# Optimization experiments

Measured on AMD Instinct MI355X. Metric: run time of the kernel, lower is better.

The kernel has to match this reference:

```python
import jax, jax.numpy as jnp
import numpy as np

B, N, D, E, K = 4, 4096, 768, 8, 2
H = 4 * D
LN_EPS = 1e-5


def setup_inputs() -> dict:
    key = jax.random.key(0)
    ks = jax.random.split(key, 9)
    s_d = 1.0 / np.sqrt(D)
    s_h = 1.0 / np.sqrt(H)
    return {
        "x": jax.random.normal(ks[0], (B, N, D), dtype=jnp.float32),
        "router_w": jax.random.normal(ks[1], (D, E), dtype=jnp.float32) * s_d,
        "router_b": jnp.zeros((E,), dtype=jnp.float32),
        "w1": jax.random.normal(ks[2], (E, D, H), dtype=jnp.float32) * s_d,
        "b1": jnp.zeros((E, H), dtype=jnp.float32),
        "w2": jax.random.normal(ks[3], (E, H, D), dtype=jnp.float32) * s_h,
        "b2": jnp.zeros((E, D), dtype=jnp.float32),
        "gamma": jnp.ones((D,), dtype=jnp.float32),
        "beta": jnp.zeros((D,), dtype=jnp.float32),
    }


def reference(x, router_w, router_b, w1, b1, w2, b2, gamma, beta):
    # Router logits and top-k gating (softmax over top-k values, in fp32)
    logits = jnp.einsum("bnd,de->bne", x, router_w) + router_b
    topv, topi = jax.lax.top_k(logits, K)                       # [B,N,K]
    w = jax.nn.softmax(topv.astype(jnp.float32), axis=-1).astype(x.dtype)
    # Per-token per-expert combine weight: [B,N,E]
    onehot = (topi[..., None] == jnp.arange(E)).astype(x.dtype)  # [B,N,K,E]
    we = jnp.einsum("bnk,bnke->bne", w, onehot)
    # Dense per-expert FFN, weighted combine (loop over small fixed E)
    out = jnp.zeros_like(x)
    for e in range(E):
        h = jax.nn.gelu(jnp.einsum("bnd,dh->bnh", x, w1[e]) + b1[e],
                        approximate=False)                      # exact GELU like torch
        y_e = jnp.einsum("bnh,hd->bnd", h, w2[e]) + b2[e]
        out = out + y_e * we[..., e:e + 1]
    # Residual + LayerNorm
    y = x + out
    mu = jnp.mean(y, axis=-1, keepdims=True)
    var = jnp.mean((y - mu) ** 2, axis=-1, keepdims=True)
    return (y - mu) * jax.lax.rsqrt(var + LN_EPS) * gamma + beta
```

## Files before the change

kernel.cpp:

```cpp
#include <hip/hip_runtime.h>
#include <hip/hip_bf16.h>
#include <math.h>

#define T_TOK 16384
#define DIM 768
#define NE 8
#define HID 3072
#define PADT 33792
#define CHUNK_CAP 16896
#define NSLOT (T_TOK * 2)

typedef unsigned short u16;
typedef __attribute__((ext_vector_type(8))) short bf16x8;
typedef __attribute__((ext_vector_type(4))) float f32x4;

__device__ __forceinline__ u16 f2bf(float f) {
  union { float f; unsigned u; } v; v.f = f;
  unsigned r = v.u + 0x7FFF + ((v.u >> 16) & 1);
  return (u16)(r >> 16);
}

__device__ __forceinline__ float bf2f(u16 u) {
  union { unsigned u; float f; } v; v.u = ((unsigned)u) << 16; return v.f;
}

__device__ __forceinline__ void async16(void* lds, const void* g) {
  __builtin_amdgcn_global_load_lds((const __attribute__((address_space(1))) void*)g,
                                   (__attribute__((address_space(3))) void*)lds, 16, 0, 0);
}

__device__ __forceinline__ float gelu_f(float v) {
  float z = fabsf(v) * 0.70710678118f;
  float t = __builtin_amdgcn_rcpf(1.f + 0.3275911f * z);
  float p = t * (0.254829592f +
            t * (-0.284496736f +
            t * (1.421413741f +
            t * (-1.453152027f +
            t * 1.061405429f))));
  float e = __expf(-z * z);
  float erfz = fmaf(-p, e, 1.f);
  float s = copysignf(erfz, v);
  return 0.5f * v * (1.f + s);
}

__global__ __launch_bounds__(256) void transpose_cvt(const float* __restrict__ in,
                                                     u16* __restrict__ outp, int R, int C) {
  __shared__ float tile[32][33];
  int e = blockIdx.z;
  int c0 = blockIdx.x * 32, r0 = blockIdx.y * 32;
  int tx = threadIdx.x & 31, ty = threadIdx.x >> 5;
  const float* ip = in + (size_t)e * R * C;
  u16* op = outp + (size_t)e * R * C;
#pragma unroll
  for (int i = 0; i < 4; ++i)
    tile[ty + i * 8][tx] = ip[(size_t)(r0 + ty + i * 8) * C + c0 + tx];
  __syncthreads();
#pragma unroll
  for (int i = 0; i < 4; ++i)
    op[(size_t)(c0 + ty + i * 8) * R + r0 + tx] = f2bf(tile[tx][ty + i * 8]);
}

__global__ __launch_bounds__(256) void router_kernel(
    const float* __restrict__ x, const float* __restrict__ rw,
    const float* __restrict__ rb, int* __restrict__ idxb,
    float* __restrict__ wtb, u16* __restrict__ xb) {
  __shared__ float rwt[NE * DIM];
  for (int i = threadIdx.x; i < NE * DIM; i += 256) {
    int d = i >> 3, e = i & 7;
    rwt[e * DIM + d] = rw[i];
  }
  __syncthreads();
  int lane = threadIdx.x & 63, wv = threadIdx.x >> 6;
#pragma unroll 1
  for (int it = 0; it < 8; ++it) {
    int t = blockIdx.x * 32 + wv * 8 + it;
    const float4* xr = (const float4*)(x + (size_t)t * DIM);
    float4 xv[3];
#pragma unroll
    for (int i = 0; i < 3; ++i) xv[i] = xr[lane + i * 64];
    ushort4* xo = (ushort4*)(xb + (size_t)t * DIM);
#pragma unroll
    for (int i = 0; i < 3; ++i)
      xo[lane + i * 64] = make_ushort4(f2bf(xv[i].x), f2bf(xv[i].y), f2bf(xv[i].z), f2bf(xv[i].w));
    float acc[NE];
#pragma unroll
    for (int e = 0; e < NE; ++e) acc[e] = 0.f;
#pragma unroll
    for (int i = 0; i < 3; ++i) {
#pragma unroll
      for (int e = 0; e < NE; ++e) {
        float4 w4 = ((const float4*)(rwt + e * DIM))[lane + i * 64];
        acc[e] += xv[i].x * w4.x + xv[i].y * w4.y + xv[i].z * w4.z + xv[i].w * w4.w;
      }
    }
#pragma unroll
    for (int e = 0; e < NE; ++e)
      for (int off = 32; off; off >>= 1) acc[e] += __shfl_down(acc[e], off);
    if (lane == 0) {
      float lg[NE];
#pragma unroll
      for (int e = 0; e < NE; ++e) lg[e] = acc[e] + rb[e];
      int i0 = 0;
#pragma unroll
      for (int e = 1; e < NE; ++e) if (lg[e] > lg[i0]) i0 = e;
      int i1 = -1;
#pragma unroll
      for (int e = 0; e < NE; ++e)
        if (e != i0 && (i1 < 0 || lg[e] > lg[i1])) i1 = e;
      float ee = expf(lg[i1] - lg[i0]);
      float w0 = 1.f / (1.f + ee);
      float w1 = ee / (1.f + ee);
      idxb[t * 2] = i0; idxb[t * 2 + 1] = i1;
      wtb[t * 2] = w0; wtb[t * 2 + 1] = w1;
    }
  }
}

__global__ __launch_bounds__(256) void hist_kernel(const int* __restrict__ idxb,
                                                   int* __restrict__ whist) {
  int wv = threadIdx.x >> 6, lane = threadIdx.x & 63;
  int g = blockIdx.x * 4 + wv;
  int cnt = 0;
#pragma unroll
  for (int j = 0; j < 2; ++j) {
    int e = idxb[g * 128 + j * 64 + lane];
#pragma unroll
    for (int ex = 0; ex < NE; ++ex) {
      unsigned long long m = __ballot(e == ex);
      if (lane == ex) cnt += __popcll(m);
    }
  }
  if (lane < NE) whist[g * NE + lane] = cnt;
}

__global__ __launch_bounds__(256) void scan_kernel(const int* __restrict__ whist,
                                                   int* __restrict__ gbase,
                                                   int* __restrict__ offsets,
                                                   int* __restrict__ counts) {
  __shared__ int sgb[256 * NE];
  __shared__ int tot[NE], soff[NE + 1];
  int tid = threadIdx.x;
  if (tid < NE) {
    int run = 0;
    for (int g = 0; g < 256; ++g) { sgb[g * NE + tid] = run; run += whist[g * NE + tid]; }
    tot[tid] = run; counts[tid] = run;
  }
  __syncthreads();
  if (tid == 0) {
    int off = 0;
    for (int e = 0; e < NE; ++e) {
      soff[e] = off; offsets[e] = off;
      off += (tot[e] + 127) & ~127;
    }
    soff[NE] = off; offsets[NE] = off;
  }
  __syncthreads();
  for (int i = tid; i < 256 * NE; i += 256) gbase[i] = sgb[i] + soff[i & 7];
}

__global__ __launch_bounds__(256) void scatter_kernel(
    const int* __restrict__ idxb, const int* __restrict__ gbase,
    int* __restrict__ g_tok, int* __restrict__ pairpos) {
  int wv = threadIdx.x >> 6, lane = threadIdx.x & 63;
  int g = blockIdx.x * 4 + wv;
  int run = (lane < NE) ? gbase[g * NE + lane] : 0;
  unsigned long long ltm = (1ull << lane) - 1ull;
#pragma unroll
  for (int j = 0; j < 2; ++j) {
    int slot = g * 128 + j * 64 + lane;
    int e = idxb[slot];
    int myrank = 0;
#pragma unroll
    for (int ex = 0; ex < NE; ++ex) {
      unsigned long long m = __ballot(e == ex);
      int b = __shfl(run, ex);
      if (e == ex) myrank = b + __popcll(m & ltm);
      if (lane == ex) run += __popcll(m);
    }
    g_tok[myrank] = slot >> 1;
    pairpos[slot] = myrank;
  }
}

__global__ __launch_bounds__(256, 2) void gemm1_kernel(
    const u16* __restrict__ xb, const u16* __restrict__ w1t,
    const float* __restrict__ b1, const int* __restrict__ g_tok,
    const int* __restrict__ offsets, const int* __restrict__ counts,
    u16* __restrict__ hbuf, int g0) {
  const int g = g0 + blockIdx.y * 128;
  int e = -1;
#pragma unroll
  for (int i = 0; i < NE; ++i)
    if (g >= offsets[i] && g < offsets[i + 1]) e = i;
  if (e < 0) return;
  const int off = offsets[e];
  const int cnt = counts[e];
  const int r0 = g - off;
  if (r0 >= cnt) return;
  const int n0 = blockIdx.x * 128;

  __shared__ u16 As[2][128 * 64];
  __shared__ u16 Bs[2][128 * 64];

  const int tid = threadIdx.x;
  const int lane = tid & 63;
  const int wv = tid >> 6;
  const int wr = wv >> 1, wc = wv & 1;
  const int scol = (((lane & 7) ^ (lane >> 3)) * 8);

  const u16* agp[4];
  const u16* bgp[4];
#pragma unroll
  for (int i = 0; i < 4; ++i) {
    int r = r0 + wv * 32 + i * 8 + (lane >> 3);
    int rr = r < cnt ? r : cnt - 1;
    int tok = g_tok[off + rr];
    agp[i] = xb + (size_t)tok * DIM + scol;
    int n = n0 + wv * 32 + i * 8 + (lane >> 3);
    bgp[i] = w1t + ((size_t)e * HID + n) * DIM + scol;
  }

  f32x4 acc[4][4];
#pragma unroll
  for (int i = 0; i < 4; ++i)
#pragma unroll
    for (int j = 0; j < 4; ++j) acc[i][j] = (f32x4){0.f, 0.f, 0.f, 0.f};

  const int NT = DIM / 64;
#pragma unroll
  for (int i = 0; i < 4; ++i) {
    async16(&As[0][(wv * 32 + i * 8) * 64], agp[i]);
    async16(&Bs[0][(wv * 32 + i * 8) * 64], bgp[i]);
  }
#pragma unroll 1
  for (int t = 0; t < NT; ++t) {
    const int cur = t & 1;
    if (t + 1 < NT) {
      const int nxt = cur ^ 1;
      const int kt = (t + 1) * 64;
#pragma unroll
      for (int i = 0; i < 4; ++i) {
        async16(&As[nxt][(wv * 32 + i * 8) * 64], agp[i] + kt);
        async16(&Bs[nxt][(wv * 32 + i * 8) * 64], bgp[i] + kt);
      }
      asm volatile("s_waitcnt vmcnt(8)" ::: "memory");
    } else {
      asm volatile("s_waitcnt vmcnt(0)" ::: "memory");
    }
    __builtin_amdgcn_s_barrier();
    __builtin_amdgcn_s_setprio(1);
#pragma unroll
    for (int kk = 0; kk < 2; ++kk) {
      bf16x8 af[4], bfr[4];
#pragma unroll
      for (int i = 0; i < 4; ++i)
        af[i] = *(const bf16x8*)&As[cur][(wr * 64 + i * 16 + (lane & 15)) * 64 +
                                        (((kk * 4 + (lane >> 4)) ^ (lane & 7)) * 8)];
#pragma unroll
      for (int j = 0; j < 4; ++j)
        bfr[j] = *(const bf16x8*)&Bs[cur][(wc * 64 + j * 16 + (lane & 15)) * 64 +
                                         (((kk * 4 + (lane >> 4)) ^ (lane & 7)) * 8)];
#pragma unroll
      for (int i = 0; i < 4; ++i)
#pragma unroll
        for (int j = 0; j < 4; ++j)
          acc[i][j] = __builtin_amdgcn_mfma_f32_16x16x32_bf16(af[i], bfr[j], acc[i][j], 0, 0, 0);
    }
    __builtin_amdgcn_s_setprio(0);
    asm volatile("" ::: "memory");
    __builtin_amdgcn_s_barrier();
  }

#pragma unroll
  for (int i = 0; i < 4; ++i) {
#pragma unroll
    for (int j = 0; j < 4; ++j) {
      int col = n0 + wc * 64 + j * 16 + (lane & 15);
      float bias = b1[e * HID + col];
#pragma unroll
      for (int rg = 0; rg < 4; ++rg) {
        int rloc = wr * 64 + i * 16 + (lane >> 4) * 4 + rg;
        if (r0 + rloc < cnt) {
          float v = gelu_f(acc[i][j][rg] + bias);
          hbuf[(size_t)(g - g0 + rloc) * HID + col] = f2bf(v);
        }
      }
    }
  }
}

__global__ __launch_bounds__(256, 2) void gemm2_kernel(
    const u16* __restrict__ hbuf, const u16* __restrict__ w2t,
    const float* __restrict__ b2, const int* __restrict__ offsets,
    const int* __restrict__ counts, u16* __restrict__ ygb, int g0) {
  const int g = g0 + blockIdx.y * 128;
  int e = -1;
#pragma unroll
  for (int i = 0; i < NE; ++i)
    if (g >= offsets[i] && g < offsets[i + 1]) e = i;
  if (e < 0) return;
  const int off = offsets[e];
  const int cnt = counts[e];
  const int r0 = g - off;
  if (r0 >= cnt) return;
  const int n0 = blockIdx.x * 128;

  __shared__ u16 As[2][128 * 64];
  __shared__ u16 Bs[2][128 * 64];

  const int tid = threadIdx.x;
  const int lane = tid & 63;
  const int wv = tid >> 6;
  const int wr = wv >> 1, wc = wv & 1;
  const int scol = (((lane & 7) ^ (lane >> 3)) * 8);

  const u16* agp[4];
  const u16* bgp[4];
#pragma unroll
  for (int i = 0; i < 4; ++i) {
    int r = r0 + wv * 32 + i * 8 + (lane >> 3);
    int rr = r < cnt ? r : cnt - 1;
    agp[i] = hbuf + (size_t)(off + rr - g0) * HID + scol;
    int n = n0 + wv * 32 + i * 8 + (lane >> 3);
    bgp[i] = w2t + ((size_t)e * DIM + n) * HID + scol;
  }

  f32x4 acc[4][4];
#pragma unroll
  for (int i = 0; i < 4; ++i)
#pragma unroll
    for (int j = 0; j < 4; ++j) acc[i][j] = (f32x4){0.f, 0.f, 0.f, 0.f};

  const int NT = HID / 64;
#pragma unroll
  for (int i = 0; i < 4; ++i) {
    async16(&As[0][(wv * 32 + i * 8) * 64], agp[i]);
    async16(&Bs[0][(wv * 32 + i * 8) * 64], bgp[i]);
  }
#pragma unroll 1
  for (int t = 0; t < NT; ++t) {
    const int cur = t & 1;
    if (t + 1 < NT) {
      const int nxt = cur ^ 1;
      const int kt = (t + 1) * 64;
#pragma unroll
      for (int i = 0; i < 4; ++i) {
        async16(&As[nxt][(wv * 32 + i * 8) * 64], agp[i] + kt);
        async16(&Bs[nxt][(wv * 32 + i * 8) * 64], bgp[i] + kt);
      }
      asm volatile("s_waitcnt vmcnt(8)" ::: "memory");
    } else {
      asm volatile("s_waitcnt vmcnt(0)" ::: "memory");
    }
    __builtin_amdgcn_s_barrier();
    __builtin_amdgcn_s_setprio(1);
#pragma unroll
    for (int kk = 0; kk < 2; ++kk) {
      bf16x8 af[4], bfr[4];
#pragma unroll
      for (int i = 0; i < 4; ++i)
        af[i] = *(const bf16x8*)&As[cur][(wr * 64 + i * 16 + (lane & 15)) * 64 +
                                        (((kk * 4 + (lane >> 4)) ^ (lane & 7)) * 8)];
#pragma unroll
      for (int j = 0; j < 4; ++j)
        bfr[j] = *(const bf16x8*)&Bs[cur][(wc * 64 + j * 16 + (lane & 15)) * 64 +
                                         (((kk * 4 + (lane >> 4)) ^ (lane & 7)) * 8)];
#pragma unroll
      for (int i = 0; i < 4; ++i)
#pragma unroll
        for (int j = 0; j < 4; ++j)
          acc[i][j] = __builtin_amdgcn_mfma_f32_16x16x32_bf16(af[i], bfr[j], acc[i][j], 0, 0, 0);
    }
    __builtin_amdgcn_s_setprio(0);
    asm volatile("" ::: "memory");
    __builtin_amdgcn_s_barrier();
  }

#pragma unroll
  for (int i = 0; i < 4; ++i) {
#pragma unroll
    for (int j = 0; j < 4; ++j) {
      int col = n0 + wc * 64 + j * 16 + (lane & 15);
      float bias = b2[e * DIM + col];
#pragma unroll
      for (int rg = 0; rg < 4; ++rg) {
        int rloc = wr * 64 + i * 16 + (lane >> 4) * 4 + rg;
        if (r0 + rloc < cnt)
          ygb[(size_t)(off + r0 + rloc) * DIM + col] = f2bf(acc[i][j][rg] + bias);
      }
    }
  }
}

__global__ __launch_bounds__(256) void combine_ln_kernel(
    const float* __restrict__ x, const u16* __restrict__ ygb,
    const int* __restrict__ pairpos, const float* __restrict__ wtb,
    const float* __restrict__ gamma, const float* __restrict__ beta,
    float* __restrict__ out) {
  int t = blockIdx.x;
  int p0 = pairpos[t * 2], p1 = pairpos[t * 2 + 1];
  float w0 = wtb[t * 2], w1 = wtb[t * 2 + 1];
  const float* xr = x + (size_t)t * DIM;
  const u16* y0 = ygb + (size_t)p0 * DIM;
  const u16* y1 = ygb + (size_t)p1 * DIM;
  float y[3];
  float s = 0.f, s2 = 0.f;
#pragma unroll
  for (int i = 0; i < 3; ++i) {
    int d = threadIdx.x + i * 256;
    float v = xr[d] + w0 * bf2f(y0[d]) + w1 * bf2f(y1[d]);
    y[i] = v; s += v; s2 += v * v;
  }
  for (int o = 32; o; o >>= 1) { s += __shfl_down(s, o); s2 += __shfl_down(s2, o); }
  __shared__ float red[8];
  int lane = threadIdx.x & 63, wv = threadIdx.x >> 6;
  if (lane == 0) { red[wv] = s; red[4 + wv] = s2; }
  __syncthreads();
  s = red[0] + red[1] + red[2] + red[3];
  s2 = red[4] + red[5] + red[6] + red[7];
  float mu = s * (1.f / DIM);
  float var = s2 * (1.f / DIM) - mu * mu;
  float inv = 1.f / sqrtf(var + 1e-5f);
#pragma unroll
  for (int i = 0; i < 3; ++i) {
    int d = threadIdx.x + i * 256;
    out[(size_t)t * DIM + d] = (y[i] - mu) * inv * gamma[d] + beta[d];
  }
}

extern "C" void kernel_launch(void* const* d_in, const int* in_sizes, int n_in,
                              void* d_out, int out_size, void* d_ws, size_t ws_size,
                              hipStream_t stream) {
  const float* x = (const float*)d_in[0];
  const float* rw = (const float*)d_in[1];
  const float* rb = (const float*)d_in[2];
  const float* w1 = (const float*)d_in[3];
  const float* b1 = (const float*)d_in[4];
  const float* w2 = (const float*)d_in[5];
  const float* b2 = (const float*)d_in[6];
  const float* gamma = (const float*)d_in[7];
  const float* beta = (const float*)d_in[8];
  float* out = (float*)d_out;

  char* p = (char*)d_ws;
  size_t o = 0;
  auto take = [&](size_t b) { void* q = (void*)(p + o); o += (b + 255) & ~((size_t)255); return q; };
  u16* xb = (u16*)take((size_t)T_TOK * DIM * 2);
  u16* w1t = (u16*)take((size_t)NE * HID * DIM * 2);
  u16* w2t = (u16*)take((size_t)NE * DIM * HID * 2);
  u16* ygb = (u16*)take((size_t)PADT * DIM * 2);
  int* g_tok = (int*)take((size_t)PADT * 4);
  int* pairpos = (int*)take((size_t)NSLOT * 4);
  int* idxb = (int*)take((size_t)NSLOT * 4);
  float* wtb = (float*)take((size_t)NSLOT * 4);
  int* whist = (int*)take((size_t)256 * NE * 4);
  int* gbase = (int*)take((size_t)256 * NE * 4);
  int* counts = (int*)take(64);
  int* offsets = (int*)take(64);
  (void)in_sizes; (void)n_in; (void)out_size;

  if (o + 256 > ws_size) return;
  size_t rem = ws_size - o;
  int chunk = (int)(rem / ((size_t)HID * 2));
  if (chunk > CHUNK_CAP) chunk = CHUNK_CAP;
  chunk &= ~127;
  if (chunk < 128) return;
  u16* hbuf = (u16*)take((size_t)chunk * HID * 2);

  router_kernel<<<512, 256, 0, stream>>>(x, rw, rb, idxb, wtb, xb);
  transpose_cvt<<<dim3(HID / 32, DIM / 32, NE), 256, 0, stream>>>(w1, w1t, DIM, HID);
  transpose_cvt<<<dim3(DIM / 32, HID / 32, NE), 256, 0, stream>>>(w2, w2t, HID, DIM);
  hist_kernel<<<64, 256, 0, stream>>>(idxb, whist);
  scan_kernel<<<1, 256, 0, stream>>>(whist, gbase, offsets, counts);
  scatter_kernel<<<64, 256, 0, stream>>>(idxb, gbase, g_tok, pairpos);
  for (int g0 = 0; g0 < PADT; g0 += chunk) {
    gemm1_kernel<<<dim3(HID / 128, chunk / 128), 256, 0, stream>>>(
        xb, w1t, b1, g_tok, offsets, counts, hbuf, g0);
    gemm2_kernel<<<dim3(DIM / 128, chunk / 128), 256, 0, stream>>>(
        hbuf, w2t, b2, offsets, counts, ygb, g0);
  }
  combine_ln_kernel<<<T_TOK, 256, 0, stream>>>(x, ygb, pairpos, wtb, gamma, beta, out);
}
```

Measured before the change: 704.5 us.

## Use 256x128 tiles with 8 waves and triple-buffered LDS pipeline in expert GEMMs

Both grouped GEMMs move from 128x128 tiles with 4 waves and double buffering to 256x128 tiles with 8 waves and a three-stage async LDS pipeline that prefetches two k-tiles ahead. B fragments are loaded once per k-tile and reused across the M sub-tiles. Expert padding becomes 256 rows and the hbuf chunk cap is raised so a single pass can cover the whole padded range. The intent is more reuse of weight tiles and more latency hiding. The cost is more LDS per block (144 KB), lower occupancy of 1 block per CU, and extra padded rows per expert.

```diff
diff --git a/kernel.cpp b/kernel.cpp
--- a/kernel.cpp
+++ b/kernel.cpp
@@ -6,8 +6,7 @@
 #define DIM 768
 #define NE 8
 #define HID 3072
-#define PADT 33792
-#define CHUNK_CAP 16896
+#define PADT 34816
 #define NSLOT (T_TOK * 2)
 
 typedef unsigned short u16;
@@ -150,7 +149,7 @@
     int off = 0;
     for (int e = 0; e < NE; ++e) {
       soff[e] = off; offsets[e] = off;
-      off += (tot[e] + 127) & ~127;
+      off += (tot[e] + 255) & ~255;
     }
     soff[NE] = off; offsets[NE] = off;
   }
@@ -182,43 +181,44 @@
   }
 }
 
-__global__ __launch_bounds__(256, 2) void gemm1_kernel(
+
+__global__ __launch_bounds__(512, 1) void gemm1_kernel(
     const u16* __restrict__ xb, const u16* __restrict__ w1t,
     const float* __restrict__ b1, const int* __restrict__ g_tok,
     const int* __restrict__ offsets, const int* __restrict__ counts,
     u16* __restrict__ hbuf, int g0) {
-  const int g = g0 + blockIdx.y * 128;
+  const int g = g0 + blockIdx.y * 256;
   int e = -1;
 #pragma unroll
   for (int i = 0; i < NE; ++i)
     if (g >= offsets[i] && g < offsets[i + 1]) e = i;
   if (e < 0) return;
-  const int off = offsets[e];
-  const int cnt = counts[e];
-  const int r0 = g - off;
+  const int off = offsets[e], cnt = counts[e], r0 = g - off;
   if (r0 >= cnt) return;
   const int n0 = blockIdx.x * 128;
 
-  __shared__ u16 As[2][128 * 64];
-  __shared__ u16 Bs[2][128 * 64];
+  __shared__ u16 As[3][256 * 64];
+  __shared__ u16 Bs[3][128 * 64];
 
   const int tid = threadIdx.x;
   const int lane = tid & 63;
-  const int wv = tid >> 6;
-  const int wr = wv >> 1, wc = wv & 1;
-  const int scol = (((lane & 7) ^ (lane >> 3)) * 8);
-
-  const u16* agp[4];
-  const u16* bgp[4];
+  const int w = tid >> 6;
+  const int wm = w >> 1;
+  const int wn = w & 1;
+  const int src = ((lane & 7) ^ (lane >> 3)) * 8;
+  const int lrow = w * 8 + (lane >> 3);
+
+  const u16* ap[4];
+  const u16* bp[2];
 #pragma unroll
   for (int i = 0; i < 4; ++i) {
-    int r = r0 + wv * 32 + i * 8 + (lane >> 3);
+    int r = r0 + i * 64 + lrow;
     int rr = r < cnt ? r : cnt - 1;
-    int tok = g_tok[off + rr];
-    agp[i] = xb + (size_t)tok * DIM + scol;
-    int n = n0 + wv * 32 + i * 8 + (lane >> 3);
-    bgp[i] = w1t + ((size_t)e * HID + n) * DIM + scol;
-  }
+    ap[i] = xb + (size_t)g_tok[off + rr] * DIM + src;
+  }
+#pragma unroll
+  for (int i = 0; i < 2; ++i)
+    bp[i] = w1t + ((size_t)e * HID + n0 + i * 64 + lrow) * DIM + src;
 
   f32x4 acc[4][4];
 #pragma unroll
@@ -227,103 +227,104 @@
     for (int j = 0; j < 4; ++j) acc[i][j] = (f32x4){0.f, 0.f, 0.f, 0.f};
 
   const int NT = DIM / 64;
-#pragma unroll
-  for (int i = 0; i < 4; ++i) {
-    async16(&As[0][(wv * 32 + i * 8) * 64], agp[i]);
-    async16(&Bs[0][(wv * 32 + i * 8) * 64], bgp[i]);
-  }
+  auto stage = [&](int buf, int kt) {
+#pragma unroll
+    for (int i = 0; i < 4; ++i)
+      async16(&As[buf][(i * 64 + w * 8) * 64], ap[i] + kt * 64);
+#pragma unroll
+    for (int i = 0; i < 2; ++i)
+      async16(&Bs[buf][(i * 64 + w * 8) * 64], bp[i] + kt * 64);
+  };
+  stage(0, 0);
+  stage(1, 1);
+  asm volatile("s_waitcnt vmcnt(6)" ::: "memory");
+  __builtin_amdgcn_s_barrier();
+
 #pragma unroll 1
   for (int t = 0; t < NT; ++t) {
-    const int cur = t & 1;
+    const int bc = t % 3;
+    if (t + 2 < NT) stage((t + 2) % 3, t + 2);
+    bf16x8 bfr[4][2];
+#pragma unroll
+    for (int nj = 0; nj < 4; ++nj)
+#pragma unroll
+      for (int kk = 0; kk < 2; ++kk)
+        bfr[nj][kk] = *(const bf16x8*)&Bs[bc][(wn * 64 + nj * 16 + (lane & 15)) * 64 +
+                                             (((kk * 4 + (lane >> 4)) ^ (lane & 7)) * 8)];
+    __builtin_amdgcn_s_setprio(1);
+#pragma unroll
+    for (int mi = 0; mi < 4; ++mi) {
+      bf16x8 af[2];
+#pragma unroll
+      for (int kk = 0; kk < 2; ++kk)
+        af[kk] = *(const bf16x8*)&As[bc][(wm * 64 + mi * 16 + (lane & 15)) * 64 +
+                                         (((kk * 4 + (lane >> 4)) ^ (lane & 7)) * 8)];
+#pragma unroll
+      for (int nj = 0; nj < 4; ++nj)
+#pragma unroll
+        for (int kk = 0; kk < 2; ++kk)
+          acc[mi][nj] = __builtin_amdgcn_mfma_f32_16x16x32_bf16(af[kk], bfr[nj][kk],
+                                                                acc[mi][nj], 0, 0, 0);
+    }
+    __builtin_amdgcn_s_setprio(0);
     if (t + 1 < NT) {
-      const int nxt = cur ^ 1;
-      const int kt = (t + 1) * 64;
-#pragma unroll
-      for (int i = 0; i < 4; ++i) {
-        async16(&As[nxt][(wv * 32 + i * 8) * 64], agp[i] + kt);
-        async16(&Bs[nxt][(wv * 32 + i * 8) * 64], bgp[i] + kt);
+      if (t + 2 < NT) asm volatile("s_waitcnt vmcnt(6)" ::: "memory");
+      else            asm volatile("s_waitcnt vmcnt(0)" ::: "memory");
+      __builtin_amdgcn_s_barrier();
+    }
+  }
+
+#pragma unroll
+  for (int mi = 0; mi < 4; ++mi)
+#pragma unroll
+    for (int nj = 0; nj < 4; ++nj) {
+      int col = n0 + wn * 64 + nj * 16 + (lane & 15);
+      float bias = b1[e * HID + col];
+#pragma unroll
+      for (int rg = 0; rg < 4; ++rg) {
+        int rloc = wm * 64 + mi * 16 + (lane >> 4) * 4 + rg;
+        if (r0 + rloc < cnt)
+          hbuf[(size_t)(g - g0 + rloc) * HID + col] = f2bf(gelu_f(acc[mi][nj][rg] + bias));
       }
-      asm volatile("s_waitcnt vmcnt(8)" ::: "memory");
-    } else {
-      asm volatile("s_waitcnt vmcnt(0)" ::: "memory");
-    }
-    __builtin_amdgcn_s_barrier();
-    __builtin_amdgcn_s_setprio(1);
-#pragma unroll
-    for (int kk = 0; kk < 2; ++kk) {
-      bf16x8 af[4], bfr[4];
-#pragma unroll
-      for (int i = 0; i < 4; ++i)
-        af[i] = *(const bf16x8*)&As[cur][(wr * 64 + i * 16 + (lane & 15)) * 64 +
-                                        (((kk * 4 + (lane >> 4)) ^ (lane & 7)) * 8)];
-#pragma unroll
-      for (int j = 0; j < 4; ++j)
-        bfr[j] = *(const bf16x8*)&Bs[cur][(wc * 64 + j * 16 + (lane & 15)) * 64 +
-                                         (((kk * 4 + (lane >> 4)) ^ (lane & 7)) * 8)];
-#pragma unroll
-      for (int i = 0; i < 4; ++i)
-#pragma unroll
-        for (int j = 0; j < 4; ++j)
-          acc[i][j] = __builtin_amdgcn_mfma_f32_16x16x32_bf16(af[i], bfr[j], acc[i][j], 0, 0, 0);
-    }
-    __builtin_amdgcn_s_setprio(0);
-    asm volatile("" ::: "memory");
-    __builtin_amdgcn_s_barrier();
-  }
-
-#pragma unroll
-  for (int i = 0; i < 4; ++i) {
-#pragma unroll
-    for (int j = 0; j < 4; ++j) {
-      int col = n0 + wc * 64 + j * 16 + (lane & 15);
-      float bias = b1[e * HID + col];
-#pragma unroll
-      for (int rg = 0; rg < 4; ++rg) {
-        int rloc = wr * 64 + i * 16 + (lane >> 4) * 4 + rg;
-        if (r0 + rloc < cnt) {
-          float v = gelu_f(acc[i][j][rg] + bias);
-          hbuf[(size_t)(g - g0 + rloc) * HID + col] = f2bf(v);
-        }
-      }
-    }
-  }
-}
-
-__global__ __launch_bounds__(256, 2) void gemm2_kernel(
+    }
+}
+
+__global__ __launch_bounds__(512, 1) void gemm2_kernel(
     const u16* __restrict__ hbuf, const u16* __restrict__ w2t,
     const float* __restrict__ b2, const int* __restrict__ offsets,
     const int* __restrict__ counts, u16* __restrict__ ygb, int g0) {
-  const int g = g0 + blockIdx.y * 128;
+  const int g = g0 + blockIdx.y * 256;
   int e = -1;
 #pragma unroll
   for (int i = 0; i < NE; ++i)
     if (g >= offsets[i] && g < offsets[i + 1]) e = i;
   if (e < 0) return;
-  const int off = offsets[e];
-  const int cnt = counts[e];
-  const int r0 = g - off;
+  const int off = offsets[e], cnt = counts[e], r0 = g - off;
   if (r0 >= cnt) return;
   const int n0 = blockIdx.x * 128;
 
-  __shared__ u16 As[2][128 * 64];
-  __shared__ u16 Bs[2][128 * 64];
+  __shared__ u16 As[3][256 * 64];
+  __shared__ u16 Bs[3][128 * 64];
 
   const int tid = threadIdx.x;
   const int lane = tid & 63;
-  const int wv = tid >> 6;
-  const int wr = wv >> 1, wc = wv & 1;
-  const int scol = (((lane & 7) ^ (lane >> 3)) * 8);
-
-  const u16* agp[4];
-  const u16* bgp[4];
+  const int w = tid >> 6;
+  const int wm = w >> 1;
+  const int wn = w & 1;
+  const int src = ((lane & 7) ^ (lane >> 3)) * 8;
+  const int lrow = w * 8 + (lane >> 3);
+
+  const u16* ap[4];
+  const u16* bp[2];
 #pragma unroll
   for (int i = 0; i < 4; ++i) {
-    int r = r0 + wv * 32 + i * 8 + (lane >> 3);
+    int r = r0 + i * 64 + lrow;
     int rr = r < cnt ? r : cnt - 1;
-    agp[i] = hbuf + (size_t)(off + rr - g0) * HID + scol;
-    int n = n0 + wv * 32 + i * 8 + (lane >> 3);
-    bgp[i] = w2t + ((size_t)e * DIM + n) * HID + scol;
-  }
+    ap[i] = hbuf + (size_t)(off + rr - g0) * HID + src;
+  }
+#pragma unroll
+  for (int i = 0; i < 2; ++i)
+    bp[i] = w2t + ((size_t)e * DIM + n0 + i * 64 + lrow) * HID + src;
 
   f32x4 acc[4][4];
 #pragma unroll
@@ -332,64 +333,66 @@
     for (int j = 0; j < 4; ++j) acc[i][j] = (f32x4){0.f, 0.f, 0.f, 0.f};
 
   const int NT = HID / 64;
-#pragma unroll
-  for (int i = 0; i < 4; ++i) {
-    async16(&As[0][(wv * 32 + i * 8) * 64], agp[i]);
-    async16(&Bs[0][(wv * 32 + i * 8) * 64], bgp[i]);
-  }
+  auto stage = [&](int buf, int kt) {
+#pragma unroll
+    for (int i = 0; i < 4; ++i)
+      async16(&As[buf][(i * 64 + w * 8) * 64], ap[i] + kt * 64);
+#pragma unroll
+    for (int i = 0; i < 2; ++i)
+      async16(&Bs[buf][(i * 64 + w * 8) * 64], bp[i] + kt * 64);
+  };
+  stage(0, 0);
+  stage(1, 1);
+  asm volatile("s_waitcnt vmcnt(6)" ::: "memory");
+  __builtin_amdgcn_s_barrier();
+
 #pragma unroll 1
   for (int t = 0; t < NT; ++t) {
-    const int cur = t & 1;
+    const int bc = t % 3;
+    if (t + 2 < NT) stage((t + 2) % 3, t + 2);
+    bf16x8 bfr[4][2];
+#pragma unroll
+    for (int nj = 0; nj < 4; ++nj)
+#pragma unroll
+      for (int kk = 0; kk < 2; ++kk)
+        bfr[nj][kk] = *(const bf16x8*)&Bs[bc][(wn * 64 + nj * 16 + (lane & 15)) * 64 +
+                                             (((kk * 4 + (lane >> 4)) ^ (lane & 7)) * 8)];
+    __builtin_amdgcn_s_setprio(1);
+#pragma unroll
+    for (int mi = 0; mi < 4; ++mi) {
+      bf16x8 af[2];
+#pragma unroll
+      for (int kk = 0; kk < 2; ++kk)
+        af[kk] = *(const bf16x8*)&As[bc][(wm * 64 + mi * 16 + (lane & 15)) * 64 +
+                                         (((kk * 4 + (lane >> 4)) ^ (lane & 7)) * 8)];
+#pragma unroll
+      for (int nj = 0; nj < 4; ++nj)
+#pragma unroll
+        for (int kk = 0; kk < 2; ++kk)
+          acc[mi][nj] = __builtin_amdgcn_mfma_f32_16x16x32_bf16(af[kk], bfr[nj][kk],
+                                                                acc[mi][nj], 0, 0, 0);
+    }
+    __builtin_amdgcn_s_setprio(0);
     if (t + 1 < NT) {
-      const int nxt = cur ^ 1;
-      const int kt = (t + 1) * 64;
-#pragma unroll
-      for (int i = 0; i < 4; ++i) {
-        async16(&As[nxt][(wv * 32 + i * 8) * 64], agp[i] + kt);
-        async16(&Bs[nxt][(wv * 32 + i * 8) * 64], bgp[i] + kt);
+      if (t + 2 < NT) asm volatile("s_waitcnt vmcnt(6)" ::: "memory");
+      else            asm volatile("s_waitcnt vmcnt(0)" ::: "memory");
+      __builtin_amdgcn_s_barrier();
+    }
+  }
+
+#pragma unroll
+  for (int mi = 0; mi < 4; ++mi)
+#pragma unroll
+    for (int nj = 0; nj < 4; ++nj) {
+      int col = n0 + wn * 64 + nj * 16 + (lane & 15);
+      float bias = b2[e * DIM + col];
+#pragma unroll
+      for (int rg = 0; rg < 4; ++rg) {
+        int rloc = wm * 64 + mi * 16 + (lane >> 4) * 4 + rg;
+        if (r0 + rloc < cnt)
+          ygb[(size_t)(g + rloc) * DIM + col] = f2bf(acc[mi][nj][rg] + bias);
       }
-      asm volatile("s_waitcnt vmcnt(8)" ::: "memory");
-    } else {
-      asm volatile("s_waitcnt vmcnt(0)" ::: "memory");
-    }
-    __builtin_amdgcn_s_barrier();
-    __builtin_amdgcn_s_setprio(1);
-#pragma unroll
-    for (int kk = 0; kk < 2; ++kk) {
-      bf16x8 af[4], bfr[4];
-#pragma unroll
-      for (int i = 0; i < 4; ++i)
-        af[i] = *(const bf16x8*)&As[cur][(wr * 64 + i * 16 + (lane & 15)) * 64 +
-                                        (((kk * 4 + (lane >> 4)) ^ (lane & 7)) * 8)];
-#pragma unroll
-      for (int j = 0; j < 4; ++j)
-        bfr[j] = *(const bf16x8*)&Bs[cur][(wc * 64 + j * 16 + (lane & 15)) * 64 +
-                                         (((kk * 4 + (lane >> 4)) ^ (lane & 7)) * 8)];
-#pragma unroll
-      for (int i = 0; i < 4; ++i)
-#pragma unroll
-        for (int j = 0; j < 4; ++j)
-          acc[i][j] = __builtin_amdgcn_mfma_f32_16x16x32_bf16(af[i], bfr[j], acc[i][j], 0, 0, 0);
-    }
-    __builtin_amdgcn_s_setprio(0);
-    asm volatile("" ::: "memory");
-    __builtin_amdgcn_s_barrier();
-  }
-
-#pragma unroll
-  for (int i = 0; i < 4; ++i) {
-#pragma unroll
-    for (int j = 0; j < 4; ++j) {
-      int col = n0 + wc * 64 + j * 16 + (lane & 15);
-      float bias = b2[e * DIM + col];
-#pragma unroll
-      for (int rg = 0; rg < 4; ++rg) {
-        int rloc = wr * 64 + i * 16 + (lane >> 4) * 4 + rg;
-        if (r0 + rloc < cnt)
-          ygb[(size_t)(off + r0 + rloc) * DIM + col] = f2bf(acc[i][j][rg] + bias);
-      }
-    }
-  }
+    }
 }
 
 __global__ __launch_bounds__(256) void combine_ln_kernel(
@@ -462,9 +465,9 @@
   if (o + 256 > ws_size) return;
   size_t rem = ws_size - o;
   int chunk = (int)(rem / ((size_t)HID * 2));
-  if (chunk > CHUNK_CAP) chunk = CHUNK_CAP;
-  chunk &= ~127;
-  if (chunk < 128) return;
+  if (chunk > PADT) chunk = PADT;
+  chunk &= ~255;
+  if (chunk < 256) return;
   u16* hbuf = (u16*)take((size_t)chunk * HID * 2);
 
   router_kernel<<<512, 256, 0, stream>>>(x, rw, rb, idxb, wtb, xb);
@@ -474,9 +477,10 @@
   scan_kernel<<<1, 256, 0, stream>>>(whist, gbase, offsets, counts);
   scatter_kernel<<<64, 256, 0, stream>>>(idxb, gbase, g_tok, pairpos);
   for (int g0 = 0; g0 < PADT; g0 += chunk) {
-    gemm1_kernel<<<dim3(HID / 128, chunk / 128), 256, 0, stream>>>(
+    int nrow = chunk / 256;
+    gemm1_kernel<<<dim3(HID / 128, nrow), 512, 0, stream>>>(
         xb, w1t, b1, g_tok, offsets, counts, hbuf, g0);
-    gemm2_kernel<<<dim3(DIM / 128, chunk / 128), 256, 0, stream>>>(
+    gemm2_kernel<<<dim3(DIM / 128, nrow), 512, 0, stream>>>(
         hbuf, w2t, b2, offsets, counts, ygb, g0);
   }
   combine_ln_kernel<<<T_TOK, 256, 0, stream>>>(x, ygb, pairpos, wtb, gamma, beta, out);
```

New measurement: 785.6 us. 11.5% more time.
